# Optimization experiments

Hardware: AMD Instinct MI355X
Metric: run time of the kernel (lower is better)

Reference implementation:

```python
import jax, jax.numpy as jnp
import numpy as np

IMG_H, IMG_W = 512.0, 512.0
PRE_NMS = 2000   # training-mode pre_nms_top_n
POST_NMS = 2000  # training-mode post_nms_top_n
NMS_THRESH = 0.7
SCORE_THRESH = 0.0
MIN_SIZE = 0.001


def setup_inputs() -> dict:
    key = jax.random.key(0)
    k1, k2, k3 = jax.random.split(key, 3)
    N = 8
    num_anchors_per_level = (49152, 12288, 3072, 768, 192)  # strides 4..64, 3 anchors/loc on 512^2
    A = sum(num_anchors_per_level)
    cxy = jax.random.uniform(k1, (N, A, 2), minval=0.0, maxval=512.0)
    wh = jax.random.uniform(k2, (N, A, 2), minval=2.0, maxval=120.0)
    proposals = jnp.concatenate([cxy - wh / 2, cxy + wh / 2], axis=-1)  # xyxy
    objectness = jax.random.normal(k3, (N, A), dtype=jnp.float32)
    return {"proposals": proposals, "objectness": objectness,
            "num_anchors_per_level": num_anchors_per_level}


def _box_iou(a, b):
    # a: [K,4], b: [K,4] -> [K,K] pairwise IoU (torchvision box_iou semantics)
    area_a = (a[:, 2] - a[:, 0]) * (a[:, 3] - a[:, 1])
    area_b = (b[:, 2] - b[:, 0]) * (b[:, 3] - b[:, 1])
    lt = jnp.maximum(a[:, None, :2], b[None, :, :2])
    rb = jnp.minimum(a[:, None, 2:], b[None, :, 2:])
    wh = jnp.clip(rb - lt, 0.0)
    inter = wh[..., 0] * wh[..., 1]
    return inter / (area_a[:, None] + area_b[None, :] - inter)


def _per_image(boxes, scores, lvl):
    # boxes [K,4] xyxy, scores [K] (sigmoid probs), lvl [K] int32 level ids
    # 1) clip to image
    x = jnp.clip(boxes[:, 0::2], 0.0, IMG_W)
    y = jnp.clip(boxes[:, 1::2], 0.0, IMG_H)
    boxes = jnp.stack([x[:, 0], y[:, 0], x[:, 1], y[:, 1]], axis=-1)
    # 2) small-box + 3) score-threshold masks (masking instead of boolean indexing)
    ws = boxes[:, 2] - boxes[:, 0]
    hs = boxes[:, 3] - boxes[:, 1]
    valid = (ws >= MIN_SIZE) & (hs >= MIN_SIZE) & (scores >= SCORE_THRESH)
    # 4) batched NMS: offset boxes per level so levels never overlap
    off = lvl.astype(boxes.dtype) * (jnp.max(boxes) + 1.0)
    off_boxes = boxes + off[:, None]
    sm = jnp.where(valid, scores, -jnp.inf)
    order = jnp.argsort(-sm)                 # descending score, invalid last
    boxes_s = boxes[order]
    scores_s = scores[order]
    valid_s = valid[order]
    ob_s = jax.lax.stop_gradient(off_boxes[order])
    K = ob_s.shape[0]
    iou = _box_iou(ob_s, ob_s)               # [K,K], keep decision is non-differentiable
    j = jnp.arange(K)
    def body(i, keep):
        suppress = keep[i] & (iou[i] > NMS_THRESH) & (j > i)
        return keep & ~suppress
    keep = jax.lax.fori_loop(0, K, body, valid_s)
    # 5) top post_nms kept boxes, padded to fixed size with zeros
    rank = jnp.cumsum(keep.astype(jnp.int32)) - 1
    sel_key = jnp.where(keep & (rank < POST_NMS), rank, K)
    idx = jnp.argsort(sel_key)[:POST_NMS]
    out_valid = sel_key[idx] < K
    out_boxes = jnp.where(out_valid[:, None], boxes_s[idx], 0.0)
    out_scores = jnp.where(out_valid, scores_s[idx], 0.0)
    return out_boxes, out_scores


def _forward(proposals, objectness, num_anchors_per_level):
    N = proposals.shape[0]
    napl = [int(n) for n in num_anchors_per_level]
    # per-level, per-image top-k on objectness (get_top_n_idx)
    idx_list, lv_list, off = [], [], 0
    for i, n in enumerate(napl):
        k = min(PRE_NMS, n)
        _, ti = jax.lax.top_k(objectness[:, off:off + n], k)
        idx_list.append(ti + off)
        lv_list.append(jnp.full((k,), i, dtype=jnp.int32))
        off += n
    top_idx = jnp.concatenate(idx_list, axis=1)   # [N, K_total]
    lvls = jnp.concatenate(lv_list)               # [K_total], same for every image
    bidx = jnp.arange(N)[:, None]
    obj = objectness[bidx, top_idx]
    props = proposals[bidx, top_idx]
    scores = jax.nn.sigmoid(obj)
    return jax.vmap(lambda b, s: _per_image(b, s, lvls))(props, scores)


def reference(proposals, objectness, num_anchors_per_level):
    # returns (boxes [N, POST_NMS, 4], scores [N, POST_NMS]); invalid slots zero-padded
    return _forward(proposals, objectness, num_anchors_per_level)
```

## Files before the change

kernel.cpp:

```cpp
#include <hip/hip_runtime.h>
#include <math.h>

#define NIMG 8
#define ATOT 65472
#define KTOT 6960
#define POST 2000
#define TILES_PER_IMG 1668
#define NTILES (NIMG*TILES_PER_IMG)
#define ESEG 1024
#define M_TIE 0.7000000178813934326171875
#define PAD(i) ((i) + ((i) >> 5))
#define WAVE_SYNC() asm volatile("s_waitcnt lgkmcnt(0)" ::: "memory")

__constant__ int c_NAPL[5]  = {49152,12288,3072,768,192};
__constant__ int c_LOFF[5]  = {0,49152,61440,64512,65280};
__constant__ int c_KSEL[5]  = {2000,2000,2000,768,192};
__constant__ int c_CBASE[5] = {0,2000,4000,6000,6768};
__constant__ int c_GLVL[5]  = {32,32,32,12,3};
__constant__ int c_TILEPFX[6] = {0,528,1056,1584,1662,1668};

typedef float v2f __attribute__((ext_vector_type(2)));

__device__ __forceinline__ v2f vmin2(v2f a, v2f b){
#if __has_builtin(__builtin_elementwise_min)
  return __builtin_elementwise_min(a, b);
#else
  v2f r; r.x = fminf(a.x, b.x); r.y = fminf(a.y, b.y); return r;
#endif
}
__device__ __forceinline__ v2f vmax2(v2f a, v2f b){
#if __has_builtin(__builtin_elementwise_max)
  return __builtin_elementwise_max(a, b);
#else
  v2f r; r.x = fmaxf(a.x, b.x); r.y = fmaxf(a.y, b.y); return r;
#endif
}

__device__ __forceinline__ unsigned f2u(float f){
  unsigned b = __float_as_uint(f);
  return (b & 0x80000000u) ? ~b : (b | 0x80000000u);
}
__device__ __forceinline__ unsigned long long mkkey(unsigned u, unsigned gidx){
  return ((unsigned long long)u << 32) | (unsigned long long)(0xFFFFFFFFu - gidx);
}
__device__ __forceinline__ unsigned long long shflx64(unsigned long long v, int m){
  int lo = __shfl_xor((int)(unsigned)v, m);
  int hi = __shfl_xor((int)(unsigned)(v >> 32), m);
  return ((unsigned long long)(unsigned)hi << 32) | (unsigned)lo;
}
__device__ __forceinline__ unsigned long long bstep(unsigned long long v, int elem,
                                                    int size, int st){
  unsigned long long p = shflx64(v, st);
  bool lower = (elem & st) == 0;
  bool desc  = (elem & size) == 0;
  bool takeMax = (lower == desc);
  bool gt = v > p;
  return (takeMax == gt) ? v : p;
}
__device__ __forceinline__ unsigned wsuffix(unsigned v, int lane){
  #pragma unroll
  for (int off = 1; off < 64; off <<= 1){
    unsigned p = __shfl_down(v, off);
    if (lane + off < 64) v += p;
  }
  return v;
}

extern "C" __global__ void __launch_bounds__(1024)
k_select(const float* __restrict__ prop, const float* __restrict__ obj,
         unsigned long long* __restrict__ cand, float4* __restrict__ cbox,
         unsigned* __restrict__ zzone){
  __shared__ unsigned long long sb[2112];
  __shared__ unsigned hist[4096];
  __shared__ unsigned h8[256];
  __shared__ unsigned wsum[16];
  __shared__ unsigned s_b12, s_cumAbove, s_t20, s_cnt;
  int task = blockIdx.x, img = task/5, lvl = task%5;
  int n = c_NAPL[lvl], k = c_KSEL[lvl], tid = threadIdx.x;
  int lane = tid & 63, wv = tid >> 6;
  if (task == 0)
    for (int i = tid; i < 1280; i += 1024) zzone[i] = 0u;

  const float4* o4 = (const float4*)(obj + (size_t)img*ATOT + c_LOFF[lvl]);
  int n4 = n >> 2;
  unsigned kk = (unsigned)k;
  unsigned T = 0u;
  if (k < n){
    for (int i = tid; i < 4096; i += 1024) hist[i] = 0u;
    if (tid < 256) h8[tid] = 0u;
    __syncthreads();
    for (int i = tid; i < n4; i += 1024){
      float4 v = o4[i];
      atomicAdd(&hist[f2u(v.x) >> 20], 1u);
      atomicAdd(&hist[f2u(v.y) >> 20], 1u);
      atomicAdd(&hist[f2u(v.z) >> 20], 1u);
      atomicAdd(&hist[f2u(v.w) >> 20], 1u);
    }
    __syncthreads();
    unsigned own[4]; unsigned s = 0;
    int b0 = tid*4;
    #pragma unroll
    for (int j = 0; j < 4; ++j){ own[j] = hist[b0+j]; s += own[j]; }
    {
      unsigned suf = wsuffix(s, lane);
      unsigned wtot = __shfl(suf, 0);
      if (lane == 0) wsum[wv] = wtot;
      __syncthreads();
      unsigned above = 0;
      for (int w2 = wv + 1; w2 < 16; ++w2) above += wsum[w2];
      unsigned suf_incl = suf + above;
      unsigned sufn = suf_incl - s;
      #pragma unroll
      for (int j = 3; j >= 0; --j){
        unsigned sufj = sufn + own[j];
        if (sufj >= kk && sufn < kk){ s_b12 = (unsigned)(b0 + j); s_cumAbove = sufn; }
        sufn = sufj;
      }
    }
    __syncthreads();
    unsigned b12 = s_b12;
    for (int i = tid; i < n4; i += 1024){
      float4 v = o4[i];
      unsigned ux = f2u(v.x), uy = f2u(v.y), uz = f2u(v.z), uw = f2u(v.w);
      if ((ux >> 20) == b12) atomicAdd(&h8[(ux >> 12) & 255u], 1u);
      if ((uy >> 20) == b12) atomicAdd(&h8[(uy >> 12) & 255u], 1u);
      if ((uz >> 20) == b12) atomicAdd(&h8[(uz >> 12) & 255u], 1u);
      if ((uw >> 20) == b12) atomicAdd(&h8[(uw >> 12) & 255u], 1u);
    }
    __syncthreads();
    {
      unsigned hval = 0, suf8 = 0;
      if (tid < 256){
        hval = h8[tid];
        suf8 = wsuffix(hval, lane);
        if (lane == 0) wsum[wv] = suf8;
      }
      __syncthreads();
      if (tid < 256){
        unsigned above = 0;
        for (int w2 = wv + 1; w2 < 4; ++w2) above += wsum[w2];
        unsigned suf_incl = suf8 + above;
        unsigned cum = s_cumAbove;
        unsigned sufj = cum + suf_incl;
        unsigned sufn = cum + (suf_incl - hval);
        if (sufj >= kk && sufn < kk) s_t20 = (s_b12 << 8) | (unsigned)tid;
      }
    }
    __syncthreads();
    T = s_t20;
  }
  if (tid == 0) s_cnt = 0u;
  __syncthreads();
  int abase = c_LOFF[lvl];
  for (int i = tid; i < n4; i += 1024){
    float4 v = o4[i];
    float vv[4] = {v.x, v.y, v.z, v.w};
    #pragma unroll
    for (int c2 = 0; c2 < 4; ++c2){
      unsigned u = f2u(vv[c2]);
      bool pred = (u >> 12) >= T;
      unsigned long long bm = __ballot(pred);
      unsigned cw = (unsigned)__popcll(bm);
      unsigned basep = 0;
      if (lane == 0 && cw) basep = atomicAdd(&s_cnt, cw);
      basep = __shfl(basep, 0);
      if (pred){
        unsigned p = basep + (unsigned)__popcll(bm & ((1ull << lane) - 1ull));
        if (p < 2048u) sb[PAD(p)] = mkkey(u, (unsigned)(abase + i*4 + c2));
      }
    }
  }
  __syncthreads();
  int cnt = (int)min(s_cnt, 2048u);
  int m = 256; while (m < k || m < cnt) m <<= 1;
  for (int i = cnt + tid; i < m; i += 1024) sb[PAD(i)] = 0ull;
  __syncthreads();

  int elemA = (wv << 7) | lane, elemB = elemA | 64;
  bool active = (elemA < m);
  unsigned long long va = 0ull, vb = 0ull;
  if (active){ va = sb[PAD(elemA)]; vb = sb[PAD(elemB)]; }
  if (active){
    for (int size = 2; size <= 64; size <<= 1)
      for (int st = size >> 1; st >= 1; st >>= 1){
        va = bstep(va, elemA, size, st);
        vb = bstep(vb, elemB, size, st);
      }
    {
      bool desc = ((elemA & 128) == 0);
      unsigned long long mx = (va > vb) ? va : vb;
      unsigned long long mn = (va > vb) ? vb : va;
      va = desc ? mx : mn; vb = desc ? mn : mx;
      for (int st = 32; st >= 1; st >>= 1){
        va = bstep(va, elemA, 128, st);
        vb = bstep(vb, elemB, 128, st);
      }
    }
  }
  for (int S = 256; S <= m; S <<= 1){
    if (active){ sb[PAD(elemA)] = va; sb[PAD(elemB)] = vb; }
    __syncthreads();
    for (int st = S >> 1; st >= 128; st >>= 1){
      for (int t = tid; t < (m >> 1); t += 1024){
        int lo = t & (st - 1);
        int i  = ((t - lo) << 1) + lo;
        int j  = i + st;
        bool desc = ((i & S) == 0);
        unsigned long long x = sb[PAD(i)], y = sb[PAD(j)];
        if (desc ? (x < y) : (x > y)){ sb[PAD(i)] = y; sb[PAD(j)] = x; }
      }
      __syncthreads();
    }
    if (active){
      va = sb[PAD(elemA)]; vb = sb[PAD(elemB)];
      bool desc = ((elemA & S) == 0);
      unsigned long long mx = (va > vb) ? va : vb;
      unsigned long long mn = (va > vb) ? vb : va;
      va = desc ? mx : mn; vb = desc ? mn : mx;
      for (int st = 32; st >= 1; st >>= 1){
        va = bstep(va, elemA, S, st);
        vb = bstep(vb, elemB, S, st);
      }
    }
  }
  const float4* pr = (const float4*)(prop + (size_t)img*ATOT*4);
  size_t base = (size_t)img*KTOT + c_CBASE[lvl];
  if (active){
    if (elemA < k){
      cand[base + elemA] = va;
      unsigned gidx = 0xFFFFFFFFu - (unsigned)(va & 0xFFFFFFFFull);
      float4 p = pr[gidx];
      cbox[base + elemA] = make_float4(fminf(fmaxf(p.x,0.f),512.f), fminf(fmaxf(p.y,0.f),512.f),
                                       fminf(fmaxf(p.z,0.f),512.f), fminf(fmaxf(p.w,0.f),512.f));
    }
    if (elemB < k){
      cand[base + elemB] = vb;
      unsigned gidx = 0xFFFFFFFFu - (unsigned)(vb & 0xFFFFFFFFull);
      float4 p = pr[gidx];
      cbox[base + elemB] = make_float4(fminf(fmaxf(p.x,0.f),512.f), fminf(fmaxf(p.y,0.f),512.f),
                                       fminf(fmaxf(p.z,0.f),512.f), fminf(fmaxf(p.w,0.f),512.f));
    }
  }
}

extern "C" __global__ void __launch_bounds__(256)
k_mask(const float4* __restrict__ cbox, unsigned* __restrict__ ecnt,
       unsigned* __restrict__ eseg, float4* __restrict__ out4, int out_n4){
  __shared__ float4 pairXY[4][32];
  __shared__ float4 pairZW[4][32];
  int tid = threadIdx.x, lane = tid & 63, wv = tid >> 6;
  int bid = blockIdx.x;
  if (bid < 79){
    int z = bid*256 + tid;
    if (z < out_n4) out4[z] = make_float4(0.f,0.f,0.f,0.f);
  }
  int tile = bid*4 + wv;
  int img = tile / TILES_PER_IMG, r = tile % TILES_PER_IMG;
  int lvl = 0;
  while (r >= c_TILEPFX[lvl + 1]) ++lvl;
  int t = r - c_TILEPFX[lvl];
  int G = c_GLVL[lvl], k = c_KSEL[lvl];
  int gi = 0;
  while (t >= G - gi){ t -= G - gi; ++gi; }
  int gj = gi + t;
  int task = img*5 + lvl;
  const float4* cb = cbox + (size_t)img*KTOT + c_CBASE[lvl];

  int jj = gj*64 + lane;
  float4 bb = (jj < k) ? cb[jj] : make_float4(0.f,0.f,0.f,0.f);
  float px_ = __shfl_xor(bb.x, 1), py_ = __shfl_xor(bb.y, 1);
  float pz_ = __shfl_xor(bb.z, 1), pw_ = __shfl_xor(bb.w, 1);
  int m2 = lane >> 1;
  if ((lane & 1) == 0)
    pairXY[wv][m2] = make_float4(bb.x, px_, bb.y, py_);
  else
    pairZW[wv][m2] = make_float4(pz_, bb.z, pw_, bb.w);
  WAVE_SYNC();

  int i = gi*64 + lane;
  float4 a = cb[(i < k) ? i : (k - 1)];
  float aarea = (a.z - a.x) * (a.w - a.y);
  v2f az = {a.z, a.z}, ax = {a.x, a.x}, aw = {a.w, a.w}, ay = {a.y, a.y};
  v2f aA = {aarea, aarea};
  const float4* pxy = pairXY[wv];
  const float4* pzw = pairZW[wv];
  unsigned long long word = 0ull;
  #pragma unroll
  for (int jp = 0; jp < 32; ++jp){
    float4 q1 = pxy[jp];
    float4 q2 = pzw[jp];
    v2f bx = {q1.x, q1.y}, by = {q1.z, q1.w};
    v2f bz = {q2.x, q2.y}, bw = {q2.z, q2.w};
    v2f ix = vmin2(az, bz) - vmax2(ax, bx);
    v2f iy = vmin2(aw, bw) - vmax2(ay, by);
    v2f inter = ix * iy;
    v2f bA = (bz - bx) * (bw - by);
    v2f uni = (aA + bA) - inter;
    v2f p7 = uni * 0.7f;
    int d0 = __float_as_int(inter.x) - __float_as_int(p7.x);
    int d1 = __float_as_int(inter.y) - __float_as_int(p7.y);
    bool ov0 = (ix.x > 0.f) & (iy.x > 0.f);
    bool ov1 = (ix.y > 0.f) & (iy.y > 0.f);
    bool hit0 = ov0 & (d0 > 8);
    bool hit1 = ov1 & (d1 > 8);
    bool amb0 = ov0 & ((unsigned)(d0 + 8) <= 16u);
    bool amb1 = ov1 & ((unsigned)(d1 + 8) <= 16u);
    if (__any(amb0 | amb1)){
      if (amb0 && ((double)inter.x >= M_TIE * (double)uni.x)) hit0 = true;
      if (amb1 && ((double)inter.y >= M_TIE * (double)uni.y)) hit1 = true;
    }
    word |= (hit0 ? (1ull << (2*jp)) : 0ull) | (hit1 ? (1ull << (2*jp + 1)) : 0ull);
  }
  if (i >= k) word = 0ull;
  if (gi == gj)
    word &= (lane == 63) ? 0ull : (~0ull << (lane + 1));

  int nb = __popcll(word);
  int pfx = nb;
  for (int d = 1; d < 64; d <<= 1){
    int v = __shfl_up(pfx, d);
    if (lane >= d) pfx += v;
  }
  int total = __shfl(pfx, 63);
  if (total > 0){
    unsigned base = 0;
    if (lane == 0) base = atomicAdd(&ecnt[task*32 + gi], (unsigned)total);
    base = __shfl(base, 0);
    unsigned idx = base + (unsigned)(pfx - nb);
    unsigned* ep = eseg + (size_t)(task*32 + gi)*ESEG;
    while (word){
      int j = __ffsll(word) - 1; word &= word - 1;
      if (idx < ESEG) ep[idx] = ((unsigned)i << 16) | (unsigned)(gj*64 + j);
      ++idx;
    }
  }
}

extern "C" __global__ void __launch_bounds__(1024)
k_scan(const unsigned long long* __restrict__ cand, const unsigned* __restrict__ ecnt,
       const unsigned* __restrict__ eseg, unsigned long long* __restrict__ clist,
       unsigned* __restrict__ ccnt){
  __shared__ unsigned ledge[6144];
  __shared__ unsigned soff[33], wpfx[33];
  __shared__ unsigned long long smA[32][64];
  __shared__ unsigned long long hasIw[32];
  __shared__ unsigned long long remW[32], keepW[32];
  int task = blockIdx.x, img = task / 5, lvl = task % 5;
  int k = c_KSEL[lvl], nW = c_GLVL[lvl], tid = threadIdx.x;
  int lane = tid & 63, wv = tid >> 6;

  if (tid < 32){
    unsigned e = (tid < nW) ? min(ecnt[task*32 + tid], (unsigned)ESEG) : 0u;
    unsigned pfx = e;
    #pragma unroll
    for (int d2 = 1; d2 < 32; d2 <<= 1){
      unsigned v = __shfl_up(pfx, d2);
      if (tid >= d2) pfx += v;
    }
    soff[tid] = pfx - e;
    if (tid == 31) soff[32] = pfx;
    remW[tid] = 0ull; hasIw[tid] = 0ull;
  }
  for (int i = tid; i < 32*64; i += 1024) ((unsigned long long*)smA)[i] = 0ull;
  __syncthreads();
  for (int w = wv; w < nW; w += 16){
    unsigned c = soff[w+1] - soff[w];
    const unsigned* ep = eseg + (size_t)(task*32 + w)*ESEG;
    for (unsigned e = lane; e < c; e += 64){
      unsigned p = soff[w] + e;
      unsigned ed = ep[e];
      if (p < 6144u) ledge[p] = ed;
      int i = (int)(ed >> 16), j = (int)(ed & 0xFFFFu);
      if ((j >> 6) == w){
        atomicOr(&smA[w][i & 63], 1ull << (j & 63));
        atomicOr(&hasIw[w], 1ull << (i & 63));
      }
    }
  }
  __syncthreads();

  if (tid < 64){
    for (int w = 0; w < nW; ++w){
      unsigned long long smreg = smA[w][lane];
      unsigned long long r = remW[w];
      unsigned long long x = hasIw[w] & ~r;
      WAVE_SYNC();
      while (x){
        int i = __ffsll(x) - 1;
        unsigned rlo = __builtin_amdgcn_readlane((unsigned)smreg, i);
        unsigned rhi = __builtin_amdgcn_readlane((unsigned)(smreg >> 32), i);
        unsigned long long row = ((unsigned long long)rhi << 32) | rlo;
        r |= row;
        x &= ~(1ull << i);
        x &= ~r;
      }
      if (lane == 0) remW[w] = r;
      unsigned long long keep_w = ~r;
      unsigned c = soff[w+1] - soff[w];
      if (c){
        const unsigned* ep = eseg + (size_t)(task*32 + w)*ESEG;
        for (unsigned e = lane; e < c; e += 64){
          unsigned p = soff[w] + e;
          unsigned ed = (p < 6144u) ? ledge[p] : ep[e];
          int i = (int)(ed >> 16), j = (int)(ed & 0xFFFFu), wj = j >> 6;
          if (wj != w && ((keep_w >> (i & 63)) & 1ull))
            atomicOr(&remW[wj], 1ull << (j & 63));
        }
      }
      WAVE_SYNC();
    }
    if (lane < 32){
      unsigned long long v = 0ull;
      if (lane < nW){
        int rem = k - lane*64;
        v = (rem >= 64) ? ~0ull : ((1ull << rem) - 1ull);
      }
      keepW[lane] = v & ~remW[lane];
    }
    WAVE_SYNC();
    if (lane == 0){
      unsigned s = 0;
      for (int w = 0; w < nW; ++w){ wpfx[w] = s; s += (unsigned)__popcll(keepW[w]); }
      ccnt[task] = s;
    }
  }
  __syncthreads();
  size_t base = (size_t)img*KTOT + c_CBASE[lvl];
  for (int i = tid; i < k; i += 1024){
    unsigned long long w = keepW[i >> 6];
    if ((w >> (i & 63)) & 1ull){
      unsigned long long lowmask = (i & 63) ? ((1ull << (i & 63)) - 1ull) : 0ull;
      unsigned rank = wpfx[i >> 6] + (unsigned)__popcll(w & lowmask);
      clist[base + rank] = cand[base + i];
    }
  }
}

__device__ __forceinline__ int cntGreater(const unsigned long long* base, int len,
                                          unsigned long long x){
  int lo = 0, hi = len;
  while (lo < hi){
    int mid = (lo + hi) >> 1;
    if (base[mid] > x) lo = mid + 1; else hi = mid;
  }
  return lo;
}

extern "C" __global__ void __launch_bounds__(1024)
k_merge(const float* __restrict__ prop, const float* __restrict__ obj,
        const unsigned long long* __restrict__ clist, const unsigned* __restrict__ ccnt,
        float* __restrict__ out){
  __shared__ unsigned long long keys[KTOT];
  __shared__ int loff[6], lcnt[5];
  int img = blockIdx.x >> 3, eighth = blockIdx.x & 7, tid = threadIdx.x;
  int lane = tid & 63, wv = tid >> 6;
  if (tid < 5) lcnt[tid] = (int)ccnt[img*5 + tid];
  __syncthreads();
  if (tid == 0){
    int s = 0;
    for (int l = 0; l < 5; ++l){ loff[l] = s; s += lcnt[l]; }
    loff[5] = s;
  }
  __syncthreads();
  if (wv < 15){
    int l = wv % 5, sub = wv / 5;
    size_t gb = (size_t)img*KTOT + c_CBASE[l];
    int c = lcnt[l], lo = loff[l];
    for (int e = sub*64 + lane; e < c; e += 192) keys[lo + e] = clist[gb + e];
  }
  __syncthreads();
  const float4* pr = (const float4*)(prop + (size_t)img*ATOT*4);
  const float*  o  = obj + (size_t)img*ATOT;
  float* ob = out + (size_t)img*POST*4;
  float* os = out + (size_t)NIMG*POST*4 + (size_t)img*POST;
  int tot = loff[5];
  for (int tt = tid; ; tt += 1024){
    int t = 8*tt + eighth;
    if (t >= tot) break;
    int lvl = 0;
    while (t >= loff[lvl + 1]) ++lvl;
    unsigned long long x = keys[t];
    int pos = t - loff[lvl];
    for (int l = 0; l < 5; ++l){
      if (l == lvl) continue;
      pos += cntGreater(keys + loff[l], lcnt[l], x);
    }
    if (pos < POST){
      unsigned gidx = 0xFFFFFFFFu - (unsigned)(x & 0xFFFFFFFFull);
      float4 p = pr[gidx];
      ob[pos*4 + 0] = fminf(fmaxf(p.x, 0.f), 512.f);
      ob[pos*4 + 1] = fminf(fmaxf(p.y, 0.f), 512.f);
      ob[pos*4 + 2] = fminf(fmaxf(p.z, 0.f), 512.f);
      ob[pos*4 + 3] = fminf(fmaxf(p.w, 0.f), 512.f);
      double sgm = 1.0 / (1.0 + exp(-(double)o[gidx]));
      os[pos] = (float)sgm;
    }
  }
}

extern "C" void kernel_launch(void* const* d_in, const int* in_sizes, int n_in,
                              void* d_out, int out_size, void* d_ws, size_t ws_size,
                              hipStream_t stream){
  const float* prop = (const float*)d_in[0];
  const float* obj  = (const float*)d_in[1];
  char* ws = (char*)d_ws;
  unsigned*           ecnt = (unsigned*)(ws);
  unsigned*           ccnt = (unsigned*)(ws + 5120);
  unsigned long long* cand = (unsigned long long*)(ws + 5632);
  unsigned long long* clist= (unsigned long long*)(ws + 451072);
  float4*             cbox = (float4*)(ws + 896512);
  unsigned*           eseg = (unsigned*)(ws + 1787392);

  int out_n4 = out_size / 4;
  hipLaunchKernelGGL(k_select, dim3(40),  dim3(1024), 0, stream, prop, obj, cand, cbox, ecnt);
  hipLaunchKernelGGL(k_mask,   dim3(NTILES/4), dim3(256), 0, stream, cbox, ecnt, eseg,
                     (float4*)d_out, out_n4);
  hipLaunchKernelGGL(k_scan,   dim3(40),  dim3(1024), 0, stream, cand, ecnt, eseg, clist, ccnt);
  hipLaunchKernelGGL(k_merge,  dim3(64),  dim3(1024), 0, stream, prop, obj, clist, ccnt, (float*)d_out);
}
```

Baseline: 163.9 us.

## Process two column tiles per wave in NMS mask and defer tie checks

Each wave in the IoU-mask kernel now handles a pair of 64-column tiles in the same row block, so the row-box load, prefix scan, edge atomics and job decode are shared across twice the work and half as many waves launch. The per-iteration wave vote for near-threshold IoU cases is replaced by an ambiguity bitmask that is resolved afterwards in double precision, taking a branch out of the hot loop. Output zeroing moves from the mask kernel into the select kernel. In exchange, register use per wave rises, and odd-length rows carry one partially wasted tile.

```diff
diff --git a/kernel.cpp b/kernel.cpp
--- a/kernel.cpp
+++ b/kernel.cpp
@@ -5,8 +5,8 @@
 #define ATOT 65472
 #define KTOT 6960
 #define POST 2000
-#define TILES_PER_IMG 1668
-#define NTILES (NIMG*TILES_PER_IMG)
+#define JOBS_PER_IMG 862
+#define NJOBS (NIMG*JOBS_PER_IMG)
 #define ESEG 1024
 #define M_TIE 0.7000000178813934326171875
 #define PAD(i) ((i) + ((i) >> 5))
@@ -17,7 +17,7 @@
 __constant__ int c_KSEL[5]  = {2000,2000,2000,768,192};
 __constant__ int c_CBASE[5] = {0,2000,4000,6000,6768};
 __constant__ int c_GLVL[5]  = {32,32,32,12,3};
-__constant__ int c_TILEPFX[6] = {0,528,1056,1584,1662,1668};
+__constant__ int c_JOBPFX[6] = {0,272,544,816,858,862};
 
 typedef float v2f __attribute__((ext_vector_type(2)));
 
@@ -69,7 +69,7 @@
 extern "C" __global__ void __launch_bounds__(1024)
 k_select(const float* __restrict__ prop, const float* __restrict__ obj,
          unsigned long long* __restrict__ cand, float4* __restrict__ cbox,
-         unsigned* __restrict__ zzone){
+         unsigned* __restrict__ zzone, float4* __restrict__ out4, int out_n4){
   __shared__ unsigned long long sb[2112];
   __shared__ unsigned hist[4096];
   __shared__ unsigned h8[256];
@@ -80,6 +80,10 @@
   int lane = tid & 63, wv = tid >> 6;
   if (task == 0)
     for (int i = tid; i < 1280; i += 1024) zzone[i] = 0u;
+  {
+    int z = task*1024 + tid;
+    if (z < out_n4) out4[z] = make_float4(0.f,0.f,0.f,0.f);
+  }
 
   const float4* o4 = (const float4*)(obj + (size_t)img*ATOT + c_LOFF[lvl]);
   int n4 = n >> 2;
@@ -245,36 +249,34 @@
 
 extern "C" __global__ void __launch_bounds__(256)
 k_mask(const float4* __restrict__ cbox, unsigned* __restrict__ ecnt,
-       unsigned* __restrict__ eseg, float4* __restrict__ out4, int out_n4){
-  __shared__ float4 pairXY[4][32];
-  __shared__ float4 pairZW[4][32];
+       unsigned* __restrict__ eseg){
+  __shared__ float4 pXY[4][2][32];
+  __shared__ float4 pZW[4][2][32];
   int tid = threadIdx.x, lane = tid & 63, wv = tid >> 6;
-  int bid = blockIdx.x;
-  if (bid < 79){
-    int z = bid*256 + tid;
-    if (z < out_n4) out4[z] = make_float4(0.f,0.f,0.f,0.f);
-  }
-  int tile = bid*4 + wv;
-  int img = tile / TILES_PER_IMG, r = tile % TILES_PER_IMG;
+  int job = blockIdx.x*4 + wv;
+  int img = job / JOBS_PER_IMG, r = job % JOBS_PER_IMG;
   int lvl = 0;
-  while (r >= c_TILEPFX[lvl + 1]) ++lvl;
-  int t = r - c_TILEPFX[lvl];
+  while (r >= c_JOBPFX[lvl + 1]) ++lvl;
+  int t = r - c_JOBPFX[lvl];
   int G = c_GLVL[lvl], k = c_KSEL[lvl];
   int gi = 0;
-  while (t >= G - gi){ t -= G - gi; ++gi; }
-  int gj = gi + t;
+  while (t >= ((G - gi + 1) >> 1)){ t -= (G - gi + 1) >> 1; ++gi; }
+  int gj0 = gi + 2*t;
   int task = img*5 + lvl;
   const float4* cb = cbox + (size_t)img*KTOT + c_CBASE[lvl];
 
-  int jj = gj*64 + lane;
-  float4 bb = (jj < k) ? cb[jj] : make_float4(0.f,0.f,0.f,0.f);
-  float px_ = __shfl_xor(bb.x, 1), py_ = __shfl_xor(bb.y, 1);
-  float pz_ = __shfl_xor(bb.z, 1), pw_ = __shfl_xor(bb.w, 1);
-  int m2 = lane >> 1;
-  if ((lane & 1) == 0)
-    pairXY[wv][m2] = make_float4(bb.x, px_, bb.y, py_);
-  else
-    pairZW[wv][m2] = make_float4(pz_, bb.z, pw_, bb.w);
+  #pragma unroll
+  for (int h = 0; h < 2; ++h){
+    int jj = (gj0 + h)*64 + lane;
+    float4 bb = (jj < k) ? cb[jj] : make_float4(0.f,0.f,0.f,0.f);
+    float px_ = __shfl_xor(bb.x, 1), py_ = __shfl_xor(bb.y, 1);
+    float pz_ = __shfl_xor(bb.z, 1), pw_ = __shfl_xor(bb.w, 1);
+    int m2 = lane >> 1;
+    if ((lane & 1) == 0)
+      pXY[wv][h][m2] = make_float4(bb.x, px_, bb.y, py_);
+    else
+      pZW[wv][h][m2] = make_float4(pz_, bb.z, pw_, bb.w);
+  }
   WAVE_SYNC();
 
   int i = gi*64 + lane;
@@ -282,40 +284,61 @@
   float aarea = (a.z - a.x) * (a.w - a.y);
   v2f az = {a.z, a.z}, ax = {a.x, a.x}, aw = {a.w, a.w}, ay = {a.y, a.y};
   v2f aA = {aarea, aarea};
-  const float4* pxy = pairXY[wv];
-  const float4* pzw = pairZW[wv];
-  unsigned long long word = 0ull;
+  unsigned long long word[2] = {0ull, 0ull}, ambw[2] = {0ull, 0ull};
   #pragma unroll
-  for (int jp = 0; jp < 32; ++jp){
-    float4 q1 = pxy[jp];
-    float4 q2 = pzw[jp];
-    v2f bx = {q1.x, q1.y}, by = {q1.z, q1.w};
-    v2f bz = {q2.x, q2.y}, bw = {q2.z, q2.w};
-    v2f ix = vmin2(az, bz) - vmax2(ax, bx);
-    v2f iy = vmin2(aw, bw) - vmax2(ay, by);
-    v2f inter = ix * iy;
-    v2f bA = (bz - bx) * (bw - by);
-    v2f uni = (aA + bA) - inter;
-    v2f p7 = uni * 0.7f;
-    int d0 = __float_as_int(inter.x) - __float_as_int(p7.x);
-    int d1 = __float_as_int(inter.y) - __float_as_int(p7.y);
-    bool ov0 = (ix.x > 0.f) & (iy.x > 0.f);
-    bool ov1 = (ix.y > 0.f) & (iy.y > 0.f);
-    bool hit0 = ov0 & (d0 > 8);
-    bool hit1 = ov1 & (d1 > 8);
-    bool amb0 = ov0 & ((unsigned)(d0 + 8) <= 16u);
-    bool amb1 = ov1 & ((unsigned)(d1 + 8) <= 16u);
-    if (__any(amb0 | amb1)){
-      if (amb0 && ((double)inter.x >= M_TIE * (double)uni.x)) hit0 = true;
-      if (amb1 && ((double)inter.y >= M_TIE * (double)uni.y)) hit1 = true;
-    }
-    word |= (hit0 ? (1ull << (2*jp)) : 0ull) | (hit1 ? (1ull << (2*jp + 1)) : 0ull);
-  }
-  if (i >= k) word = 0ull;
-  if (gi == gj)
-    word &= (lane == 63) ? 0ull : (~0ull << (lane + 1));
-
-  int nb = __popcll(word);
+  for (int h = 0; h < 2; ++h){
+    const float4* pxy = pXY[wv][h];
+    const float4* pzw = pZW[wv][h];
+    #pragma unroll
+    for (int jp = 0; jp < 32; ++jp){
+      float4 q1 = pxy[jp];
+      float4 q2 = pzw[jp];
+      v2f bx = {q1.x, q1.y}, by = {q1.z, q1.w};
+      v2f bz = {q2.x, q2.y}, bw = {q2.z, q2.w};
+      v2f ix = vmin2(az, bz) - vmax2(ax, bx);
+      v2f iy = vmin2(aw, bw) - vmax2(ay, by);
+      v2f inter = ix * iy;
+      v2f bA = (bz - bx) * (bw - by);
+      v2f uni = (aA + bA) - inter;
+      v2f p7 = uni * 0.7f;
+      int d0 = __float_as_int(inter.x) - __float_as_int(p7.x);
+      int d1 = __float_as_int(inter.y) - __float_as_int(p7.y);
+      bool ov0 = (ix.x > 0.f) & (iy.x > 0.f);
+      bool ov1 = (ix.y > 0.f) & (iy.y > 0.f);
+      bool hit0 = ov0 & (d0 > 8);
+      bool hit1 = ov1 & (d1 > 8);
+      bool amb0 = ov0 & ((unsigned)(d0 + 8) <= 16u);
+      bool amb1 = ov1 & ((unsigned)(d1 + 8) <= 16u);
+      word[h] |= (hit0 ? (1ull << (2*jp)) : 0ull) | (hit1 ? (1ull << (2*jp+1)) : 0ull);
+      ambw[h] |= (amb0 ? (1ull << (2*jp)) : 0ull) | (amb1 ? (1ull << (2*jp+1)) : 0ull);
+    }
+  }
+  if (__any(ambw[0] | ambw[1])){
+    #pragma unroll
+    for (int h = 0; h < 2; ++h){
+      unsigned long long aw2 = ambw[h];
+      while (aw2){
+        int j = __ffsll(aw2) - 1; aw2 &= aw2 - 1;
+        int jp = j >> 1, comp = j & 1;
+        float4 q1 = pXY[wv][h][jp];
+        float4 q2 = pZW[wv][h][jp];
+        float bx = comp ? q1.y : q1.x, by = comp ? q1.w : q1.z;
+        float bz = comp ? q2.y : q2.x, bw = comp ? q2.w : q2.z;
+        float ix = fminf(a.z, bz) - fmaxf(a.x, bx);
+        float iy = fminf(a.w, bw) - fmaxf(a.y, by);
+        float inter = ix * iy;
+        float bA = (bz - bx) * (bw - by);
+        float uni = (aarea + bA) - inter;
+        if ((double)inter >= M_TIE * (double)uni)
+          word[h] |= (1ull << j);
+      }
+    }
+  }
+  if (i >= k){ word[0] = 0ull; word[1] = 0ull; }
+  if (gi == gj0)
+    word[0] &= (lane == 63) ? 0ull : (~0ull << (lane + 1));
+
+  int nb = __popcll(word[0]) + __popcll(word[1]);
   int pfx = nb;
   for (int d = 1; d < 64; d <<= 1){
     int v = __shfl_up(pfx, d);
@@ -328,10 +351,15 @@
     base = __shfl(base, 0);
     unsigned idx = base + (unsigned)(pfx - nb);
     unsigned* ep = eseg + (size_t)(task*32 + gi)*ESEG;
-    while (word){
-      int j = __ffsll(word) - 1; word &= word - 1;
-      if (idx < ESEG) ep[idx] = ((unsigned)i << 16) | (unsigned)(gj*64 + j);
-      ++idx;
+    #pragma unroll
+    for (int h = 0; h < 2; ++h){
+      unsigned long long w = word[h];
+      int colbase = (gj0 + h)*64;
+      while (w){
+        int j = __ffsll(w) - 1; w &= w - 1;
+        if (idx < ESEG) ep[idx] = ((unsigned)i << 16) | (unsigned)(colbase + j);
+        ++idx;
+      }
     }
   }
 }
@@ -512,9 +540,9 @@
   unsigned*           eseg = (unsigned*)(ws + 1787392);
 
   int out_n4 = out_size / 4;
-  hipLaunchKernelGGL(k_select, dim3(40),  dim3(1024), 0, stream, prop, obj, cand, cbox, ecnt);
-  hipLaunchKernelGGL(k_mask,   dim3(NTILES/4), dim3(256), 0, stream, cbox, ecnt, eseg,
-                     (float4*)d_out, out_n4);
+  hipLaunchKernelGGL(k_select, dim3(40),  dim3(1024), 0, stream, prop, obj, cand, cbox,
+                     ecnt, (float4*)d_out, out_n4);
+  hipLaunchKernelGGL(k_mask,   dim3(NJOBS/4), dim3(256), 0, stream, cbox, ecnt, eseg);
   hipLaunchKernelGGL(k_scan,   dim3(40),  dim3(1024), 0, stream, cand, ecnt, eseg, clist, ccnt);
   hipLaunchKernelGGL(k_merge,  dim3(64),  dim3(1024), 0, stream, prop, obj, clist, ccnt, (float*)d_out);
 }
```

New measurement: 163.2 us. About the same (-0.4%).
